# Kernel optimization log

Hardware: AMD Instinct MI355X
Metric: run time of the kernel (lower is better)

Reference implementation:

```python
import jax, jax.numpy as jnp
import numpy as np

B, N, E, D, H, HW, L = 16, 32, 256, 256, 8, 784, 4
DH = D // H
FF = 4 * D
BN = B * N
BE = B * E
SCALE = 1.0 / np.sqrt(DH)


def _ln(x, g, b):
    m = x.mean(-1, keepdims=True)
    v = ((x - m) ** 2).mean(-1, keepdims=True)
    return (x - m) * jax.lax.rsqrt(v + 1e-5) * g + b


def setup_inputs() -> dict:
    key = jax.random.key(0)
    ks = iter(jax.random.split(key, 64))
    def w(shape, s=0.05):
        return jax.random.normal(next(ks), shape, jnp.float32) * s
    inp = {
        'nodes': w((B, N, D), 1.0),
        'edges': w((B, E, D), 1.0),
        'images': w((B, HW, D), 1.0),
        'mask': jnp.zeros((B * H, N + E, HW), jnp.float32),
        'node_enc': w((BN, D), 1.0),
        'edge_enc': w((BE, D), 1.0),
        'ln1_g': jnp.ones((L, D), jnp.float32), 'ln1_b': jnp.zeros((L, D), jnp.float32),
        'Wqkv': w((L, D, 3 * D)), 'bqkv': jnp.zeros((L, 3 * D), jnp.float32),
        'Wo': w((L, D, D)), 'bo': jnp.zeros((L, D), jnp.float32),
        'ls1': jnp.full((L, D), 0.1, jnp.float32),
        'ln2_g': jnp.ones((L, D), jnp.float32), 'ln2_b': jnp.zeros((L, D), jnp.float32),
        'Wn1': w((L, D, D)), 'bn1': jnp.zeros((L, D), jnp.float32),
        'Wn2': w((L, D, D)), 'bn2': jnp.zeros((L, D), jnp.float32),
        'We': w((L, D, D)), 'be': jnp.zeros((L, D), jnp.float32),
        'attn_p': w((L, H, DH), 1.0),
        'Weo': w((L, D, D)), 'beo': jnp.zeros((L, D), jnp.float32),
        'Wno': w((L, D, D)), 'bno': jnp.zeros((L, D), jnp.float32),
        'ls2': jnp.full((L, D), 0.1, jnp.float32),
        'ln3_g': jnp.ones((L, D), jnp.float32), 'ln3_b': jnp.zeros((L, D), jnp.float32),
        'W1': w((L, D, FF)), 'b1': jnp.zeros((L, FF), jnp.float32),
        'W2': w((L, FF, D)), 'b2': jnp.zeros((L, D), jnp.float32),
        'ls3': jnp.full((L, D), 0.1, jnp.float32),
        'edge_index': jax.random.randint(next(ks), (2, BE), 0, BN, jnp.int32),
    }
    return inp


def reference(nodes, edges, images, mask, node_enc, edge_enc,
              ln1_g, ln1_b, Wqkv, bqkv, Wo, bo, ls1,
              ln2_g, ln2_b, Wn1, bn1, Wn2, bn2, We, be, attn_p, Weo, beo, Wno, bno, ls2,
              ln3_g, ln3_b, W1, b1, W2, b2, ls3, edge_index):
    idx0, idx1 = edge_index[0], edge_index[1]
    ne = jnp.concatenate([nodes, edges], axis=1)  # [B, N+E, D]
    mask4 = mask.reshape(B, H, N + E, HW)
    for l in range(L):
        # cross-attention ne -> images
        ne1n = _ln(ne, ln1_g[l], ln1_b[l])
        q = (ne1n @ Wqkv[l, :, :D] + bqkv[l, :D]).reshape(B, N + E, H, DH)
        k = (images @ Wqkv[l, :, D:2 * D] + bqkv[l, D:2 * D]).reshape(B, HW, H, DH)
        v = (images @ Wqkv[l, :, 2 * D:] + bqkv[l, 2 * D:]).reshape(B, HW, H, DH)
        scores = jnp.einsum('bqhd,bkhd->bhqk', q, k) * SCALE + mask4
        attn = jax.nn.softmax(scores, axis=-1)
        ctx = jnp.einsum('bhqk,bkhd->bqhd', attn, v).reshape(B, N + E, D)
        ne1 = ne + ls1[l] * (ctx @ Wo[l] + bo[l])
        # modified GAT on flattened graph
        ne2n = _ln(ne1, ln2_g[l], ln2_b[l])
        nodes_f = ne2n[:, :N].reshape(BN, D) + node_enc
        edges_f = ne2n[:, N:].reshape(BE, D) + edge_enc
        fn = (nodes_f @ Wn1[l] + bn1[l])[idx0]
        sn = (nodes_f @ Wn2[l] + bn2[l])[idx0]  # NOTE: original code uses edge_index[0] here too
        ep = edges_f @ We[l] + be[l]
        hidden = jax.nn.gelu(fn + sn + ep, approximate=False)  # [BE, D]
        pres = (hidden.reshape(BE, H, DH) * attn_p[l]).sum(-1)  # [BE, H]
        mseg = jax.ops.segment_max(pres, idx0, num_segments=BN)
        expv = jnp.exp(pres - mseg[idx0])
        denom = jax.ops.segment_sum(expv, idx0, num_segments=BN)
        alpha = expv / denom[idx0]  # scatter_softmax over destination nodes
        new_edges = hidden @ Weo[l] + beo[l]
        vals = (nodes_f[idx1] + new_edges) @ Wno[l] + bno[l]
        vals = vals.reshape(BE, H, DH) * alpha[..., None]
        new_nodes = jax.ops.segment_sum(vals.reshape(BE, D), idx0, num_segments=BN)
        gat = jnp.concatenate([new_nodes.reshape(B, N, D), new_edges.reshape(B, E, D)], axis=1)
        ne2 = ne1 + ls2[l] * gat
        # FFN
        ne3n = _ln(ne2, ln3_g[l], ln3_b[l])
        ffn = jax.nn.gelu(ne3n @ W1[l] + b1[l], approximate=False) @ W2[l] + b2[l]
        ne = ne2 + ls3[l] * ffn
    return ne
```

## Files before the change

kernel.cpp:

```cpp
#include <hip/hip_runtime.h>
#include <math.h>

static constexpr int B_  = 16;
static constexpr int N_  = 32;
static constexpr int E_  = 256;
static constexpr int D_  = 256;
static constexpr int H_  = 8;
static constexpr int HW_ = 784;
static constexpr int L_  = 4;
static constexpr int DH_ = 32;
static constexpr int FF_ = 1024;
static constexpr int BN_ = 512;
static constexpr int BE_ = 4096;
static constexpr int NE_ = 288;
static constexpr int ROWS_ = B_ * H_ * NE_;
#define SCALE_ 0.17677669529663687f

static constexpr size_t LAYER_W = 1114112;
static constexpr size_t OFF_Q   = 0;
static constexpr size_t OFF_K   = 65536;
static constexpr size_t OFF_WO  = 196608;
static constexpr size_t OFF_WN1 = 262144;
static constexpr size_t OFF_WE  = 393216;
static constexpr size_t OFF_WEO = 458752;
static constexpr size_t OFF_WNO = 524288;
static constexpr size_t OFF_W1  = 589824;
static constexpr size_t OFF_W2  = 851968;

typedef __attribute__((ext_vector_type(8))) short bf16x8;
typedef __attribute__((ext_vector_type(4))) float f32x4;

typedef __attribute__((address_space(1))) const unsigned int gas_uint;
typedef __attribute__((address_space(3))) unsigned int las_uint;

__device__ __forceinline__ void gload16(const unsigned short* g, unsigned short* lds) {
    __builtin_amdgcn_global_load_lds((gas_uint*)g, (las_uint*)lds, 16, 0, 0);
}

__device__ __forceinline__ float gelu_f(float x) {
    return 0.5f * x * (1.0f + erff(x * 0.7071067811865476f));
}

__device__ __forceinline__ unsigned short f2bf(float x) {
    unsigned u = __float_as_uint(x);
    u += 0x7FFFu + ((u >> 16) & 1u);
    return (unsigned short)(u >> 16);
}
__device__ __forceinline__ unsigned pack2bf(float a, float b) {
    return (unsigned)f2bf(a) | ((unsigned)f2bf(b) << 16);
}
__device__ __forceinline__ float bf2f(unsigned short u) {
    return __uint_as_float(((unsigned)u) << 16);
}


__global__ void concat_kernel(const float* __restrict__ nodes, const float* __restrict__ edges,
                              float* __restrict__ ne) {
    int tid = blockIdx.x * 256 + threadIdx.x;
    int d = tid & 255;
    int row = tid >> 8;
    int b = row / NE_, pos = row % NE_;
    float v = (pos < N_) ? nodes[(size_t)(b * N_ + pos) * D_ + d]
                         : edges[(size_t)(b * E_ + (pos - N_)) * D_ + d];
    ne[tid] = v;
}

__global__ void imgcast_kernel(const float* __restrict__ img, unsigned short* __restrict__ out) {
    int tid = blockIdx.x * 256 + threadIdx.x;
    const float* p = img + (size_t)tid * 8;
    float4 a = *(const float4*)(p);
    float4 b = *(const float4*)(p + 4);
    uint4 o = make_uint4(pack2bf(a.x, a.y), pack2bf(a.z, a.w),
                         pack2bf(b.x, b.y), pack2bf(b.z, b.w));
    *(uint4*)&out[(size_t)tid * 8] = o;
}

__device__ __forceinline__ float ln_from_val(float v, int d,
                                             const float* __restrict__ g, const float* __restrict__ bta,
                                             float* sh1, float* sh2) {
    float s = v, s2 = v * v;
    #pragma unroll
    for (int o = 32; o >= 1; o >>= 1) { s += __shfl_down(s, o); s2 += __shfl_down(s2, o); }
    int lane = d & 63, w = d >> 6;
    if (lane == 0) { sh1[w] = s; sh2[w] = s2; }
    __syncthreads();
    if (d == 0) {
        float a = sh1[0] + sh1[1] + sh1[2] + sh1[3];
        float c = sh2[0] + sh2[1] + sh2[2] + sh2[3];
        sh1[0] = a; sh2[0] = c;
    }
    __syncthreads();
    float mean = sh1[0] * (1.0f / D_);
    float var  = sh2[0] * (1.0f / D_) - mean * mean;
    float rstd = rsqrtf(var + 1e-5f);
    return (v - mean) * rstd * g[d] + bta[d];
}

__global__ __launch_bounds__(256) void ln_kernel(const float* __restrict__ x,
                                                 unsigned short* __restrict__ y,
                                                 const float* __restrict__ g,
                                                 const float* __restrict__ bta) {
    __shared__ float sh1[4], sh2[4];
    const int row = blockIdx.x, d = threadIdx.x;
    float v = x[(size_t)row * D_ + d];
    y[(size_t)row * D_ + d] = f2bf(ln_from_val(v, d, g, bta, sh1, sh2));
}

__global__ __launch_bounds__(256) void ln2enc_kernel(const float* __restrict__ x,
                                                     const float* __restrict__ g,
                                                     const float* __restrict__ bta,
                                                     const float* __restrict__ node_enc,
                                                     const float* __restrict__ edge_enc,
                                                     unsigned short* __restrict__ nodes_f,
                                                     unsigned short* __restrict__ edges_f) {
    __shared__ float sh1[4], sh2[4];
    const int row = blockIdx.x, d = threadIdx.x;
    float v = x[(size_t)row * D_ + d];
    float val = ln_from_val(v, d, g, bta, sh1, sh2);
    int b = row / NE_, pos = row % NE_;
    if (pos < N_) {
        int rn = b * N_ + pos;
        nodes_f[(size_t)rn * D_ + d] = f2bf(val + node_enc[(size_t)rn * D_ + d]);
    } else {
        int re = b * E_ + (pos - N_);
        edges_f[(size_t)re * D_ + d] = f2bf(val + edge_enc[(size_t)re * D_ + d]);
    }
}

__global__ __launch_bounds__(256) void gatres_ln_kernel(
    float* __restrict__ ne, const float* __restrict__ new_nodes,
    const float* __restrict__ new_edges, const float* __restrict__ ls2l,
    const float* __restrict__ g, const float* __restrict__ bta,
    unsigned short* __restrict__ lnb) {
    __shared__ float sh1[4], sh2[4];
    const int row = blockIdx.x, d = threadIdx.x;
    int b = row / NE_, pos = row % NE_;
    float gv = (pos < N_) ? new_nodes[(size_t)(b * N_ + pos) * D_ + d]
                          : new_edges[(size_t)(b * E_ + (pos - N_)) * D_ + d];
    float v = ne[(size_t)row * D_ + d] + ls2l[d] * gv;
    ne[(size_t)row * D_ + d] = v;
    lnb[(size_t)row * D_ + d] = f2bf(ln_from_val(v, d, g, bta, sh1, sh2));
}

__global__ __launch_bounds__(256) void wtrans_kernel(
    const float* __restrict__ Wqkv, const float* __restrict__ Wo,
    const float* __restrict__ Wn1,  const float* __restrict__ Wn2,
    const float* __restrict__ We,   const float* __restrict__ Weo,
    const float* __restrict__ Wno,  const float* __restrict__ W1,
    const float* __restrict__ W2,   unsigned short* __restrict__ wT)
{
    const int bid = blockIdx.x;
    const int l = bid / 1088;
    int tl = bid % 1088;
    const float* src; int ld, K, Nn; unsigned short* dst;
    if (tl < 576) {
        int mid = tl >> 6; tl &= 63;
        K = 256; Nn = 256;
        if (mid < 3) {
            src = Wqkv + (size_t)l * 256 * 768 + mid * 256; ld = 768;
            dst = wT + (size_t)l * LAYER_W + (size_t)mid * 65536;
        } else {
            const float* bases[6] = {Wo, Wn1, Wn2, We, Weo, Wno};
            src = bases[mid - 3] + (size_t)l * 65536; ld = 256;
            dst = wT + (size_t)l * LAYER_W + OFF_WO + (size_t)(mid - 3) * 65536;
        }
    } else if (tl < 832) {
        tl -= 576; K = 256; Nn = 1024;
        src = W1 + (size_t)l * 262144; ld = 1024;
        dst = wT + (size_t)l * LAYER_W + OFF_W1;
    } else {
        tl -= 832; K = 1024; Nn = 256;
        src = W2 + (size_t)l * 262144; ld = 256;
        dst = wT + (size_t)l * LAYER_W + OFF_W2;
    }
    const int ntn = Nn >> 5;
    const int k0 = (tl / ntn) << 5, n0 = (tl % ntn) << 5;
    __shared__ float ts[32][33];
    const int t = threadIdx.x;
    const int kl = t >> 5, nl = t & 31;
    #pragma unroll
    for (int rr = 0; rr < 4; ++rr)
        ts[kl + rr * 8][nl] = src[(size_t)(k0 + kl + rr * 8) * ld + n0 + nl];
    __syncthreads();
    const int onl = t >> 3, okl = (t & 7) << 2;
    ushort4 o;
    o.x = f2bf(ts[okl + 0][onl]); o.y = f2bf(ts[okl + 1][onl]);
    o.z = f2bf(ts[okl + 2][onl]); o.w = f2bf(ts[okl + 3][onl]);
    *(ushort4*)&dst[(size_t)(n0 + onl) * K + k0 + okl] = o;
}

template<int MODE, int OUTBF>
__global__ __launch_bounds__(256) void mgemm_kernel(
    const unsigned short* __restrict__ A, int lda,
    const unsigned short* __restrict__ Bt,
    const float* __restrict__ bias,
    const float* __restrict__ bias2,
    const float* __restrict__ res,
    const float* __restrict__ ls,
    void* __restrict__ Cv, int ldc, int K)
{
    __shared__ __align__(16) unsigned short As[64 * 64];
    __shared__ __align__(16) unsigned short Bs[64 * 64];
    const int m0 = blockIdx.y * 64, n0 = blockIdx.x * 64;
    const int t = threadIdx.x;
    const int l = t & 63, w = t >> 6;
    const int wr = (w >> 1) * 32, wc = (w & 1) * 32;
    const int frow = l & 15, kg = l >> 4;
    const int srow = w * 8 + (l >> 3);
    const int scolh = 8 * ((l & 7) ^ (l >> 3));
    const int ldsoff = w * 512;
    const int sw = (frow & 7) << 3;
    f32x4 acc[2][2];
    acc[0][0] = (f32x4){0.f,0.f,0.f,0.f}; acc[0][1] = acc[0][0];
    acc[1][0] = acc[0][0];                acc[1][1] = acc[0][0];
    for (int k0 = 0; k0 < K; k0 += 64) {
        const unsigned short* ga = A  + (size_t)(m0 + srow) * lda + k0 + scolh;
        const unsigned short* gb = Bt + (size_t)(n0 + srow) * K   + k0 + scolh;
        gload16(ga,                As + ldsoff);
        gload16(ga + 32 * lda,     As + ldsoff + 2048);
        gload16(gb,                Bs + ldsoff);
        gload16(gb + (size_t)32 * K, Bs + ldsoff + 2048);
        __syncthreads();
        #pragma unroll
        for (int kk = 0; kk < 2; ++kk) {
            const int off = (kk * 32 + kg * 8) ^ sw;
            bf16x8 af0 = *(const bf16x8*)&As[(wr + frow) * 64 + off];
            bf16x8 af1 = *(const bf16x8*)&As[(wr + 16 + frow) * 64 + off];
            bf16x8 bf0 = *(const bf16x8*)&Bs[(wc + frow) * 64 + off];
            bf16x8 bf1 = *(const bf16x8*)&Bs[(wc + 16 + frow) * 64 + off];
            acc[0][0] = __builtin_amdgcn_mfma_f32_16x16x32_bf16(af0, bf0, acc[0][0], 0, 0, 0);
            acc[0][1] = __builtin_amdgcn_mfma_f32_16x16x32_bf16(af0, bf1, acc[0][1], 0, 0, 0);
            acc[1][0] = __builtin_amdgcn_mfma_f32_16x16x32_bf16(af1, bf0, acc[1][0], 0, 0, 0);
            acc[1][1] = __builtin_amdgcn_mfma_f32_16x16x32_bf16(af1, bf1, acc[1][1], 0, 0, 0);
        }
        __syncthreads();
    }
    #pragma unroll
    for (int fr = 0; fr < 2; ++fr) {
        #pragma unroll
        for (int fc = 0; fc < 2; ++fc) {
            int n = n0 + wc + fc * 16 + frow;
            float bv = (bias2 != nullptr && n >= 256) ? bias2[n - 256] : bias[n];
            float lv = (MODE == 2) ? ls[n] : 0.f;
            #pragma unroll
            for (int rg = 0; rg < 4; ++rg) {
                int m = m0 + wr + fr * 16 + kg * 4 + rg;
                float vv = acc[fr][fc][rg] + bv;
                if (MODE == 1) vv = gelu_f(vv);
                if (MODE == 2) vv = res[(size_t)m * ldc + n] + lv * vv;
                if (OUTBF) ((unsigned short*)Cv)[(size_t)m * ldc + n] = f2bf(vv);
                else       ((float*)Cv)[(size_t)m * ldc + n] = vv;
            }
        }
    }
}

__global__ __launch_bounds__(128) void attn_part_kernel(
    const unsigned short* __restrict__ q, const unsigned short* __restrict__ kv,
    const float* __restrict__ mask,
    float* __restrict__ pm, float* __restrict__ pl, float* __restrict__ pO)
{
    const int bid = blockIdx.x;
    const int half = bid & 1;
    const int h = (bid >> 1) & 7;
    const int qt = (bid >> 4) % 9;
    const int b = (bid >> 4) / 9;
    const int q0 = qt * 32;
    const int t = threadIdx.x;
    const int w = t >> 6, l = t & 63;
    const int lr = l & 15, lg = l >> 4;
    const int cs = half ? 6 : 0;
    const int nc = half ? 7 : 6;

    __shared__ unsigned short Ks[2][64][40];
    __shared__ unsigned short Vs[2][32][72];
    __shared__ unsigned short Pl[2][16][72];

    bf16x8 qfrag = *(const bf16x8*)(q + ((size_t)(b * NE_ + q0 + w * 16 + lr)) * D_ + h * DH_ + lg * 8);

    const int kkey = t >> 1, kdh = (t & 1) * 16;
    const int vdh = (t & 7) * 4, vk0 = (t >> 3) * 2;
    const unsigned short* kbase = kv + ((size_t)b * HW_) * 512 + h * DH_;
    const unsigned short* vbase = kv + ((size_t)b * HW_) * 512 + 256 + h * DH_;
    const float* mbase = mask + ((size_t)(b * H_ + h) * NE_ + q0 + w * 16 + lg * 4) * (size_t)HW_;

    uint4 kq0, kq1;
    ushort4 va[2], vb4[2];
    float mreg[2][4][4];

    auto issue_kv = [&](int c0) {
        {
            int key = c0 + kkey;
            bool ok = key < HW_;
            const unsigned short* kp = kbase + (size_t)(ok ? key : 0) * 512 + kdh;
            kq0 = *(const uint4*)(kp);
            kq1 = *(const uint4*)(kp + 8);
            if (!ok) { kq0 = make_uint4(0,0,0,0); kq1 = kq0; }
        }
        #pragma unroll
        for (int r = 0; r < 2; ++r) {
            int key = c0 + vk0 + 32 * r;
            bool ok0 = key < HW_, ok1 = (key + 1) < HW_;
            const unsigned short* vp = vbase + (size_t)(ok0 ? key : 0) * 512 + vdh;
            va[r]  = *(const ushort4*)(vp);
            vb4[r] = *(const ushort4*)(vp + (ok1 ? 512 : 0));
            if (!ok0) va[r]  = make_ushort4(0,0,0,0);
            if (!ok1) vb4[r] = make_ushort4(0,0,0,0);
        }
    };
    auto write_kv = [&](int bufi) {
        *(uint4*)&Ks[bufi][kkey][kdh]     = kq0;
        *(uint4*)&Ks[bufi][kkey][kdh + 8] = kq1;
        #pragma unroll
        for (int r = 0; r < 2; ++r) {
            const unsigned short* a = (const unsigned short*)&va[r];
            const unsigned short* c = (const unsigned short*)&vb4[r];
            #pragma unroll
            for (int i = 0; i < 4; ++i)
                *(unsigned*)&Vs[bufi][vdh + i][vk0 + 32 * r] = (unsigned)a[i] | ((unsigned)c[i] << 16);
        }
    };
    auto issue_mask = [&](int c0, int set) {
        #pragma unroll
        for (int rg = 0; rg < 4; ++rg)
            #pragma unroll
            for (int fc = 0; fc < 4; ++fc) {
                int col = c0 + fc * 16 + lr;
                mreg[set][rg][fc] = (col < HW_) ? mbase[(size_t)rg * HW_ + col] : -1e30f;
            }
    };

    f32x4 oacc[2];
    oacc[0] = (f32x4){0.f, 0.f, 0.f, 0.f}; oacc[1] = oacc[0];
    float m_i[4] = {-INFINITY, -INFINITY, -INFINITY, -INFINITY};
    float l_i[4] = {0.f, 0.f, 0.f, 0.f};

    issue_kv(cs * 64);
    issue_mask(cs * 64, 0);
    write_kv(0);
    if (nc > 1) issue_mask(cs * 64 + 64, 1);
    __syncthreads();

    for (int i = 0; i < nc; ++i) {
        const int c0 = (cs + i) * 64;
        const int cb = i & 1, nb = cb ^ 1;
        const int set = i & 1;
        if (i + 1 < nc) issue_kv(c0 + 64);

        f32x4 sacc[4];
        #pragma unroll
        for (int fc = 0; fc < 4; ++fc) {
            sacc[fc] = (f32x4){0.f, 0.f, 0.f, 0.f};
            bf16x8 kf = *(const bf16x8*)&Ks[cb][fc * 16 + lr][lg * 8];
            sacc[fc] = __builtin_amdgcn_mfma_f32_16x16x32_bf16(qfrag, kf, sacc[fc], 0, 0, 0);
        }
        float s[4][4];
        #pragma unroll
        for (int fc = 0; fc < 4; ++fc)
            #pragma unroll
            for (int rg = 0; rg < 4; ++rg)
                s[fc][rg] = sacc[fc][rg] * SCALE_ + mreg[set][rg][fc];
        if (i + 2 < nc) issue_mask(c0 + 128, set);

        float mloc[4];
        #pragma unroll
        for (int rg = 0; rg < 4; ++rg)
            mloc[rg] = fmaxf(fmaxf(s[0][rg], s[1][rg]), fmaxf(s[2][rg], s[3][rg]));
        #pragma unroll
        for (int off = 1; off < 16; off <<= 1)
            #pragma unroll
            for (int rg = 0; rg < 4; ++rg)
                mloc[rg] = fmaxf(mloc[rg], __shfl_xor(mloc[rg], off));
        float scl[4], lloc[4];
        #pragma unroll
        for (int rg = 0; rg < 4; ++rg) {
            float mn = fmaxf(m_i[rg], mloc[rg]);
            scl[rg] = __expf(m_i[rg] - mn);
            m_i[rg] = mn;
        }
        #pragma unroll
        for (int rg = 0; rg < 4; ++rg) {
            float acc = 0.f;
            #pragma unroll
            for (int fc = 0; fc < 4; ++fc) {
                float p = __expf(s[fc][rg] - m_i[rg]);
                s[fc][rg] = p;
                acc += p;
            }
            lloc[rg] = acc;
        }
        #pragma unroll
        for (int off = 1; off < 16; off <<= 1)
            #pragma unroll
            for (int rg = 0; rg < 4; ++rg)
                lloc[rg] += __shfl_xor(lloc[rg], off);
        #pragma unroll
        for (int rg = 0; rg < 4; ++rg) {
            l_i[rg] = l_i[rg] * scl[rg] + lloc[rg];
            oacc[0][rg] *= scl[rg];
            oacc[1][rg] *= scl[rg];
        }

        #pragma unroll
        for (int fc = 0; fc < 4; ++fc)
            #pragma unroll
            for (int rg = 0; rg < 4; ++rg)
                Pl[w][lg * 4 + rg][fc * 16 + lr] = f2bf(s[fc][rg]);
        #pragma unroll
        for (int ks2 = 0; ks2 < 2; ++ks2) {
            bf16x8 pf = *(const bf16x8*)&Pl[w][lr][ks2 * 32 + lg * 8];
            #pragma unroll
            for (int d2 = 0; d2 < 2; ++d2) {
                bf16x8 vf = *(const bf16x8*)&Vs[cb][d2 * 16 + lr][ks2 * 32 + lg * 8];
                oacc[d2] = __builtin_amdgcn_mfma_f32_16x16x32_bf16(pf, vf, oacc[d2], 0, 0, 0);
            }
        }

        if (i + 1 < nc) {
            write_kv(nb);
            __syncthreads();
        }
    }

    const int rowbase = (b * H_ + h) * NE_ + q0 + w * 16 + lg * 4;
    #pragma unroll
    for (int rg = 0; rg < 4; ++rg) {
        size_t gr = (size_t)half * ROWS_ + rowbase + rg;
        #pragma unroll
        for (int d2 = 0; d2 < 2; ++d2)
            pO[gr * 32 + d2 * 16 + lr] = oacc[d2][rg];
        if (lr == 0) { pm[gr] = m_i[rg]; pl[gr] = l_i[rg]; }
    }
}

__global__ __launch_bounds__(256) void attn_combine_kernel(
    const float* __restrict__ pm, const float* __restrict__ pl,
    const float* __restrict__ pO, unsigned short* __restrict__ ctx)
{
    int tid = blockIdx.x * 256 + threadIdx.x;
    int row = tid >> 5, dh = tid & 31;
    float m0 = pm[row], m1 = pm[ROWS_ + row];
    float l0 = pl[row], l1 = pl[ROWS_ + row];
    float mm = fmaxf(m0, m1);
    float w0 = __expf(m0 - mm), w1 = __expf(m1 - mm);
    float L = l0 * w0 + l1 * w1;
    float o = (pO[(size_t)row * 32 + dh] * w0 + pO[((size_t)ROWS_ + row) * 32 + dh] * w1) / L;
    int bh = row / NE_, qq = row % NE_;
    int b = bh >> 3, h = bh & 7;
    ctx[((size_t)(b * NE_ + qq)) * D_ + h * DH_ + dh] = f2bf(o);
}


__global__ __launch_bounds__(256) void hidden_kernel(
    const float* __restrict__ gn12,
    unsigned short* __restrict__ hid, const int* __restrict__ idx0,
    const float* __restrict__ attn_p_l, float* __restrict__ pres) {
    int e = blockIdx.x;
    int d = threadIdx.x;
    int n = idx0[e];
    float x = bf2f(hid[(size_t)e * D_ + d]) + gn12[(size_t)n * 512 + d] + gn12[(size_t)n * 512 + 256 + d];
    float hv = gelu_f(x);
    hid[(size_t)e * D_ + d] = f2bf(hv);
    float pr = hv * attn_p_l[d];
    #pragma unroll
    for (int o = 1; o < 32; o <<= 1) pr += __shfl_xor(pr, o);
    if ((d & 31) == 0) pres[e * H_ + (d >> 5)] = pr;
}

__global__ void segsoft_kernel(const float* __restrict__ pres, const int* __restrict__ csr_off,
                               const int* __restrict__ csr_perm,
                               float* __restrict__ mseg, float* __restrict__ denom) {
    int tid = blockIdx.x * 256 + threadIdx.x;
    int n = tid >> 3, h = tid & 7;
    int s = csr_off[n], e2 = csr_off[n + 1];
    float mx = -INFINITY;
    for (int i = s; i < e2; ++i) mx = fmaxf(mx, pres[csr_perm[i] * H_ + h]);
    float sum = 0.f;
    for (int i = s; i < e2; ++i) sum += expf(pres[csr_perm[i] * H_ + h] - mx);
    mseg[tid] = mx;
    denom[tid] = sum;
}

__global__ void vin_kernel(const unsigned short* __restrict__ nodes_f,
                           const float* __restrict__ new_edges,
                           const int* __restrict__ idx1, unsigned short* __restrict__ vin) {
    int tid = blockIdx.x * 256 + threadIdx.x;
    int e = tid >> 8, d = tid & 255;
    vin[tid] = f2bf(bf2f(nodes_f[(size_t)idx1[e] * D_ + d]) + new_edges[tid]);
}

__global__ __launch_bounds__(256) void nodeagg_kernel(
    const float* __restrict__ vals, const float* __restrict__ pres,
    const float* __restrict__ mseg, const float* __restrict__ denom,
    const int* __restrict__ csr_off, const int* __restrict__ csr_perm,
    float* __restrict__ new_nodes) {
    int n = blockIdx.x;
    int d = threadIdx.x;
    int s = csr_off[n], e2 = csr_off[n + 1];
    int h = d >> 5;
    float ms = mseg[n * H_ + h];
    float rd = 1.0f / denom[n * H_ + h];
    float acc = 0.f;
    for (int i = s; i < e2; ++i) {
        int e = csr_perm[i];
        float a = expf(pres[e * H_ + h] - ms) * rd;
        acc += vals[(size_t)e * D_ + d] * a;
    }
    new_nodes[(size_t)n * D_ + d] = acc;
}


__global__ void zero_counts(int* counts) {
    int t = blockIdx.x * 256 + threadIdx.x;
    if (t < BN_) counts[t] = 0;
}

__global__ void csr_count(const int* __restrict__ idx0, int* __restrict__ counts) {
    int e = blockIdx.x * 256 + threadIdx.x;
    if (e < BE_) atomicAdd(&counts[idx0[e]], 1);
}

__global__ __launch_bounds__(512) void csr_scan(const int* __restrict__ counts, int* __restrict__ csr_off) {
    __shared__ int buf[BN_];
    int t = threadIdx.x;
    int c = counts[t];
    buf[t] = c;
    __syncthreads();
    for (int o = 1; o < BN_; o <<= 1) {
        int add = (t >= o) ? buf[t - o] : 0;
        __syncthreads();
        buf[t] += add;
        __syncthreads();
    }
    csr_off[t] = buf[t] - c;
    if (t == BN_ - 1) csr_off[BN_] = buf[t];
}

__global__ __launch_bounds__(64) void csr_fill(const int* __restrict__ idx0,
                                               const int* __restrict__ csr_off,
                                               int* __restrict__ csr_perm) {
    int n = blockIdx.x;
    int lane = threadIdx.x;
    int w = csr_off[n];
    for (int c0 = 0; c0 < BE_; c0 += 64) {
        int e = c0 + lane;
        bool m = (idx0[e] == n);
        unsigned long long bal = __ballot(m);
        if (m) {
            int pre = __popcll(bal & ((1ull << lane) - 1ull));
            csr_perm[w + pre] = e;
        }
        w += __popcll(bal);
    }
}


static void launch_mgemm(hipStream_t s, int mode, int outbf,
                         const unsigned short* A, int lda, const unsigned short* Bt,
                         const float* bias, const float* bias2, const float* res, const float* ls,
                         void* C, int ldc, int M, int N, int K) {
    dim3 g(N / 64, M / 64);
    if (mode == 0) {
        if (outbf) mgemm_kernel<0,1><<<g, 256, 0, s>>>(A, lda, Bt, bias, bias2, res, ls, C, ldc, K);
        else       mgemm_kernel<0,0><<<g, 256, 0, s>>>(A, lda, Bt, bias, bias2, res, ls, C, ldc, K);
    } else if (mode == 1) {
        mgemm_kernel<1,1><<<g, 256, 0, s>>>(A, lda, Bt, bias, bias2, res, ls, C, ldc, K);
    } else {
        mgemm_kernel<2,0><<<g, 256, 0, s>>>(A, lda, Bt, bias, bias2, res, ls, C, ldc, K);
    }
}

extern "C" void kernel_launch(void* const* d_in, const int* in_sizes, int n_in,
                              void* d_out, int out_size, void* d_ws, size_t ws_size,
                              hipStream_t stream) {
    const float* nodes    = (const float*)d_in[0];
    const float* edges    = (const float*)d_in[1];
    const float* images   = (const float*)d_in[2];
    const float* mask     = (const float*)d_in[3];
    const float* node_enc = (const float*)d_in[4];
    const float* edge_enc = (const float*)d_in[5];
    const float* ln1_g = (const float*)d_in[6];
    const float* ln1_b = (const float*)d_in[7];
    const float* Wqkv  = (const float*)d_in[8];
    const float* bqkv  = (const float*)d_in[9];
    const float* Wo    = (const float*)d_in[10];
    const float* bo    = (const float*)d_in[11];
    const float* ls1   = (const float*)d_in[12];
    const float* ln2_g = (const float*)d_in[13];
    const float* ln2_b = (const float*)d_in[14];
    const float* Wn1   = (const float*)d_in[15];
    const float* bn1   = (const float*)d_in[16];
    const float* Wn2   = (const float*)d_in[17];
    const float* bn2   = (const float*)d_in[18];
    const float* We    = (const float*)d_in[19];
    const float* be    = (const float*)d_in[20];
    const float* attn_p= (const float*)d_in[21];
    const float* Weo   = (const float*)d_in[22];
    const float* beo   = (const float*)d_in[23];
    const float* Wno   = (const float*)d_in[24];
    const float* bno   = (const float*)d_in[25];
    const float* ls2   = (const float*)d_in[26];
    const float* ln3_g = (const float*)d_in[27];
    const float* ln3_b = (const float*)d_in[28];
    const float* W1    = (const float*)d_in[29];
    const float* b1    = (const float*)d_in[30];
    const float* W2    = (const float*)d_in[31];
    const float* b2    = (const float*)d_in[32];
    const float* ls3   = (const float*)d_in[33];
    const int*   edge_index = (const int*)d_in[34];
    const int* idx0 = edge_index;
    const int* idx1 = edge_index + BE_;

    float* ne = (float*)d_out;

    float* cur = (float*)d_ws;
    auto alloc = [&](size_t nfl) { float* p = cur; cur += nfl; return p; };
    auto allocbf = [&](size_t nbf) { float* p = cur; cur += (nbf + 1) / 2; return (unsigned short*)p; };

    unsigned short* lnbuf   = allocbf((size_t)B_ * NE_ * D_);
    unsigned short* qb      = allocbf((size_t)B_ * NE_ * D_);
    unsigned short* kvb     = allocbf((size_t)B_ * HW_ * 512);
    unsigned short* ffnh    = kvb;
    unsigned short* imgbf   = allocbf((size_t)B_ * HW_ * D_);
    unsigned short* ctxb    = allocbf((size_t)B_ * NE_ * D_);
    unsigned short* nodes_f = allocbf((size_t)BN_ * D_);
    unsigned short* edges_f = allocbf((size_t)BE_ * D_);
    unsigned short* hid     = allocbf((size_t)BE_ * D_);
    unsigned short* vin     = allocbf((size_t)BE_ * D_);
    float* gn12     = alloc((size_t)BN_ * 512);
    float* pres     = alloc((size_t)BE_ * H_);
    float* mseg     = alloc((size_t)BN_ * H_);
    float* denom    = alloc((size_t)BN_ * H_);
    float* new_edges= alloc((size_t)BE_ * D_);
    float* valsb    = alloc((size_t)BE_ * D_);
    float* new_nodes= alloc((size_t)BN_ * D_);
    float* pm       = alloc((size_t)2 * ROWS_);
    float* pl       = alloc((size_t)2 * ROWS_);
    float* pO       = alloc((size_t)2 * ROWS_ * 32);
    int* counts   = (int*)cur; cur += BN_;
    int* csr_off  = (int*)cur; cur += BN_ + 4;
    int* csr_perm = (int*)cur; cur += BE_;
    cur = (float*)(((uintptr_t)cur + 255) & ~(uintptr_t)255);
    unsigned short* wT = (unsigned short*)cur;

    wtrans_kernel<<<4 * 1088, 256, 0, stream>>>(Wqkv, Wo, Wn1, Wn2, We, Weo, Wno, W1, W2, wT);
    imgcast_kernel<<<(B_ * HW_ * D_) / (256 * 8), 256, 0, stream>>>(images, imgbf);
    zero_counts<<<2, 256, 0, stream>>>(counts);
    csr_count<<<BE_ / 256, 256, 0, stream>>>(idx0, counts);
    csr_scan<<<1, 512, 0, stream>>>(counts, csr_off);
    csr_fill<<<BN_, 64, 0, stream>>>(idx0, csr_off, csr_perm);
    concat_kernel<<<(B_ * NE_ * D_) / 256, 256, 0, stream>>>(nodes, edges, ne);

    for (int l = 0; l < L_; ++l) {
        const unsigned short* wTl = wT + (size_t)l * LAYER_W;
        const float* bqkv_l = bqkv + (size_t)l * 3 * D_;

        ln_kernel<<<B_ * NE_, 256, 0, stream>>>(ne, lnbuf, ln1_g + l * D_, ln1_b + l * D_);
        launch_mgemm(stream, 0, 1, lnbuf, D_, wTl + OFF_Q, bqkv_l, nullptr, nullptr, nullptr,
                     qb, D_, B_ * NE_, D_, D_);
        launch_mgemm(stream, 0, 1, imgbf, D_, wTl + OFF_K, bqkv_l + D_, nullptr, nullptr, nullptr,
                     kvb, 512, B_ * HW_, 512, D_);
        attn_part_kernel<<<2304, 128, 0, stream>>>(qb, kvb, mask, pm, pl, pO);
        attn_combine_kernel<<<(ROWS_ * 32) / 256, 256, 0, stream>>>(pm, pl, pO, ctxb);
        launch_mgemm(stream, 2, 0, ctxb, D_, wTl + OFF_WO, bo + l * D_, nullptr, ne, ls1 + l * D_,
                     ne, D_, B_ * NE_, D_, D_);

        ln2enc_kernel<<<B_ * NE_, 256, 0, stream>>>(ne, ln2_g + l * D_, ln2_b + l * D_,
                                                    node_enc, edge_enc, nodes_f, edges_f);
        launch_mgemm(stream, 0, 0, nodes_f, D_, wTl + OFF_WN1, bn1 + l * D_, bn2 + l * D_,
                     nullptr, nullptr, gn12, 512, BN_, 512, D_);
        launch_mgemm(stream, 0, 1, edges_f, D_, wTl + OFF_WE, be + l * D_, nullptr, nullptr, nullptr,
                     hid, D_, BE_, D_, D_);
        hidden_kernel<<<BE_, 256, 0, stream>>>(gn12, hid, idx0, attn_p + (size_t)l * H_ * DH_, pres);
        segsoft_kernel<<<(BN_ * H_) / 256, 256, 0, stream>>>(pres, csr_off, csr_perm, mseg, denom);
        launch_mgemm(stream, 0, 0, hid, D_, wTl + OFF_WEO, beo + l * D_, nullptr, nullptr, nullptr,
                     new_edges, D_, BE_, D_, D_);
        vin_kernel<<<(BE_ * D_) / 256, 256, 0, stream>>>(nodes_f, new_edges, idx1, vin);
        launch_mgemm(stream, 0, 0, vin, D_, wTl + OFF_WNO, bno + l * D_, nullptr, nullptr, nullptr,
                     valsb, D_, BE_, D_, D_);
        nodeagg_kernel<<<BN_, 256, 0, stream>>>(valsb, pres, mseg, denom, csr_off, csr_perm, new_nodes);
        gatres_ln_kernel<<<B_ * NE_, 256, 0, stream>>>(ne, new_nodes, new_edges, ls2 + l * D_,
                                                       ln3_g + l * D_, ln3_b + l * D_, lnbuf);

        launch_mgemm(stream, 1, 1, lnbuf, D_, wTl + OFF_W1, b1 + l * FF_, nullptr, nullptr, nullptr,
                     ffnh, FF_, B_ * NE_, FF_, D_);
        launch_mgemm(stream, 2, 0, ffnh, FF_, wTl + OFF_W2, b2 + l * D_, nullptr, ne, ls3 + l * D_,
                     ne, D_, B_ * NE_, D_, FF_);
    }
}
```

Before: 704.4 us.

## Pre-convert mask to bf16 fragment layout once and drop split-KV attention

Adds a one-time premask kernel that converts the float32 attention mask to bf16, stored per block in the exact order each thread consumes it. All four layers' attention then read half the mask bytes with coalesced uint4 loads instead of scattered float loads. The attention kernel also stops splitting the key range in two, so each block walks all 13 key chunks and writes the normalised context directly, which removes the combine kernel and its partial buffers. The costs are half as many attention blocks (less parallelism), an extra pre-pass plus buffer, and bf16 rounding of mask values.

```diff
diff --git a/kernel.cpp b/kernel.cpp
--- a/kernel.cpp
+++ b/kernel.cpp
@@ -13,7 +13,8 @@
 static constexpr int BN_ = 512;
 static constexpr int BE_ = 4096;
 static constexpr int NE_ = 288;
-static constexpr int ROWS_ = B_ * H_ * NE_;
+static constexpr int NC_ = 13;
+static constexpr int NBLK_ = B_ * H_ * 9;
 #define SCALE_ 0.17677669529663687f
 
 static constexpr size_t LAYER_W = 1114112;
@@ -73,6 +74,47 @@
     uint4 o = make_uint4(pack2bf(a.x, a.y), pack2bf(a.z, a.w),
                          pack2bf(b.x, b.y), pack2bf(b.z, b.w));
     *(uint4*)&out[(size_t)tid * 8] = o;
+}
+
+__global__ __launch_bounds__(128) void premask_kernel(const float* __restrict__ mask,
+                                                      unsigned short* __restrict__ pmask) {
+    const int bid = blockIdx.x;
+    const int c = bid % NC_;
+    const int bq = bid / NC_;
+    const int h = bq & 7;
+    const int qt = (bq >> 3) % 9;
+    const int b = (bq >> 3) / 9;
+    const int q0 = qt * 32, c0 = c * 64;
+    __shared__ float ts[32][68];
+    const int t = threadIdx.x;
+    const int row = t >> 2, cg = (t & 3) * 16;
+    const float* mrow = mask + ((size_t)(b * H_ + h) * NE_ + q0 + row) * (size_t)HW_;
+    #pragma unroll
+    for (int i = 0; i < 4; ++i) {
+        int col = c0 + cg + i * 4;
+        float4 m4;
+        if (col + 4 <= HW_) {
+            m4 = *(const float4*)(mrow + col);
+        } else {
+            m4.x = (col + 0 < HW_) ? mrow[col + 0] : -1e30f;
+            m4.y = (col + 1 < HW_) ? mrow[col + 1] : -1e30f;
+            m4.z = (col + 2 < HW_) ? mrow[col + 2] : -1e30f;
+            m4.w = (col + 3 < HW_) ? mrow[col + 3] : -1e30f;
+        }
+        *(float4*)&ts[row][cg + i * 4] = m4;
+    }
+    __syncthreads();
+    const int w = t >> 6, lg = (t & 63) >> 4, lr = t & 15;
+    const int r0 = w * 16 + lg * 4;
+    unsigned u[8];
+    #pragma unroll
+    for (int rg = 0; rg < 4; ++rg) {
+        u[rg * 2 + 0] = pack2bf(ts[r0 + rg][0 * 16 + lr], ts[r0 + rg][1 * 16 + lr]);
+        u[rg * 2 + 1] = pack2bf(ts[r0 + rg][2 * 16 + lr], ts[r0 + rg][3 * 16 + lr]);
+    }
+    uint4* dst = (uint4*)(pmask + (size_t)bid * 2048 + t * 16);
+    dst[0] = make_uint4(u[0], u[1], u[2], u[3]);
+    dst[1] = make_uint4(u[4], u[5], u[6], u[7]);
 }
 
 __device__ __forceinline__ float ln_from_val(float v, int d,
@@ -255,22 +297,18 @@
     }
 }
 
-__global__ __launch_bounds__(128) void attn_part_kernel(
+__global__ __launch_bounds__(128) void attn_kernel(
     const unsigned short* __restrict__ q, const unsigned short* __restrict__ kv,
-    const float* __restrict__ mask,
-    float* __restrict__ pm, float* __restrict__ pl, float* __restrict__ pO)
+    const unsigned short* __restrict__ pmask, unsigned short* __restrict__ ctx)
 {
     const int bid = blockIdx.x;
-    const int half = bid & 1;
-    const int h = (bid >> 1) & 7;
-    const int qt = (bid >> 4) % 9;
-    const int b = (bid >> 4) / 9;
+    const int h = bid & 7;
+    const int qt = (bid >> 3) % 9;
+    const int b = (bid >> 3) / 9;
     const int q0 = qt * 32;
     const int t = threadIdx.x;
     const int w = t >> 6, l = t & 63;
     const int lr = l & 15, lg = l >> 4;
-    const int cs = half ? 6 : 0;
-    const int nc = half ? 7 : 6;
 
     __shared__ unsigned short Ks[2][64][40];
     __shared__ unsigned short Vs[2][32][72];
@@ -282,11 +320,11 @@
     const int vdh = (t & 7) * 4, vk0 = (t >> 3) * 2;
     const unsigned short* kbase = kv + ((size_t)b * HW_) * 512 + h * DH_;
     const unsigned short* vbase = kv + ((size_t)b * HW_) * 512 + 256 + h * DH_;
-    const float* mbase = mask + ((size_t)(b * H_ + h) * NE_ + q0 + w * 16 + lg * 4) * (size_t)HW_;
+    const uint4* mbase = (const uint4*)(pmask + (size_t)bid * NC_ * 2048 + t * 16);
 
     uint4 kq0, kq1;
     ushort4 va[2], vb4[2];
-    float mreg[2][4][4];
+    uint4 mc0, mc1, mn0, mn1;
 
     auto issue_kv = [&](int c0) {
         {
@@ -320,32 +358,22 @@
                 *(unsigned*)&Vs[bufi][vdh + i][vk0 + 32 * r] = (unsigned)a[i] | ((unsigned)c[i] << 16);
         }
     };
-    auto issue_mask = [&](int c0, int set) {
-        #pragma unroll
-        for (int rg = 0; rg < 4; ++rg)
-            #pragma unroll
-            for (int fc = 0; fc < 4; ++fc) {
-                int col = c0 + fc * 16 + lr;
-                mreg[set][rg][fc] = (col < HW_) ? mbase[(size_t)rg * HW_ + col] : -1e30f;
-            }
-    };
 
     f32x4 oacc[2];
     oacc[0] = (f32x4){0.f, 0.f, 0.f, 0.f}; oacc[1] = oacc[0];
     float m_i[4] = {-INFINITY, -INFINITY, -INFINITY, -INFINITY};
     float l_i[4] = {0.f, 0.f, 0.f, 0.f};
 
-    issue_kv(cs * 64);
-    issue_mask(cs * 64, 0);
+    issue_kv(0);
+    mc0 = mbase[0]; mc1 = mbase[1];
     write_kv(0);
-    if (nc > 1) issue_mask(cs * 64 + 64, 1);
+    mn0 = mbase[128]; mn1 = mbase[129];
     __syncthreads();
 
-    for (int i = 0; i < nc; ++i) {
-        const int c0 = (cs + i) * 64;
-        const int cb = i & 1, nb = cb ^ 1;
-        const int set = i & 1;
-        if (i + 1 < nc) issue_kv(c0 + 64);
+    for (int c = 0; c < NC_; ++c) {
+        const int c0 = c * 64;
+        const int cb = c & 1, nb = cb ^ 1;
+        if (c + 1 < NC_) issue_kv(c0 + 64);
 
         f32x4 sacc[4];
         #pragma unroll
@@ -355,12 +383,16 @@
             sacc[fc] = __builtin_amdgcn_mfma_f32_16x16x32_bf16(qfrag, kf, sacc[fc], 0, 0, 0);
         }
         float s[4][4];
-        #pragma unroll
-        for (int fc = 0; fc < 4; ++fc)
+        {
+            unsigned uw[8] = {mc0.x, mc0.y, mc0.z, mc0.w, mc1.x, mc1.y, mc1.z, mc1.w};
             #pragma unroll
-            for (int rg = 0; rg < 4; ++rg)
-                s[fc][rg] = sacc[fc][rg] * SCALE_ + mreg[set][rg][fc];
-        if (i + 2 < nc) issue_mask(c0 + 128, set);
+            for (int rg = 0; rg < 4; ++rg) {
+                s[0][rg] = sacc[0][rg] * SCALE_ + bf2f((unsigned short)(uw[rg * 2] & 0xffff));
+                s[1][rg] = sacc[1][rg] * SCALE_ + bf2f((unsigned short)(uw[rg * 2] >> 16));
+                s[2][rg] = sacc[2][rg] * SCALE_ + bf2f((unsigned short)(uw[rg * 2 + 1] & 0xffff));
+                s[3][rg] = sacc[3][rg] * SCALE_ + bf2f((unsigned short)(uw[rg * 2 + 1] >> 16));
+            }
+        }
 
         float mloc[4];
         #pragma unroll
@@ -416,38 +448,25 @@
             }
         }
 
-        if (i + 1 < nc) {
+        mc0 = mn0; mc1 = mn1;
+        if (c + 2 < NC_) {
+            mn0 = mbase[(c + 2) * 128];
+            mn1 = mbase[(c + 2) * 128 + 1];
+        }
+        if (c + 1 < NC_) {
             write_kv(nb);
             __syncthreads();
         }
     }
 
-    const int rowbase = (b * H_ + h) * NE_ + q0 + w * 16 + lg * 4;
+    unsigned short* cbase = ctx + ((size_t)(b * NE_ + q0 + w * 16 + lg * 4)) * D_ + h * DH_;
     #pragma unroll
     for (int rg = 0; rg < 4; ++rg) {
-        size_t gr = (size_t)half * ROWS_ + rowbase + rg;
+        float inv = 1.0f / l_i[rg];
         #pragma unroll
         for (int d2 = 0; d2 < 2; ++d2)
-            pO[gr * 32 + d2 * 16 + lr] = oacc[d2][rg];
-        if (lr == 0) { pm[gr] = m_i[rg]; pl[gr] = l_i[rg]; }
-    }
-}
-
-__global__ __launch_bounds__(256) void attn_combine_kernel(
-    const float* __restrict__ pm, const float* __restrict__ pl,
-    const float* __restrict__ pO, unsigned short* __restrict__ ctx)
-{
-    int tid = blockIdx.x * 256 + threadIdx.x;
-    int row = tid >> 5, dh = tid & 31;
-    float m0 = pm[row], m1 = pm[ROWS_ + row];
-    float l0 = pl[row], l1 = pl[ROWS_ + row];
-    float mm = fmaxf(m0, m1);
-    float w0 = __expf(m0 - mm), w1 = __expf(m1 - mm);
-    float L = l0 * w0 + l1 * w1;
-    float o = (pO[(size_t)row * 32 + dh] * w0 + pO[((size_t)ROWS_ + row) * 32 + dh] * w1) / L;
-    int bh = row / NE_, qq = row % NE_;
-    int b = bh >> 3, h = bh & 7;
-    ctx[((size_t)(b * NE_ + qq)) * D_ + h * DH_ + dh] = f2bf(o);
+            cbase[(size_t)rg * D_ + d2 * 16 + lr] = f2bf(oacc[d2][rg] * inv);
+    }
 }
 
 
@@ -627,6 +646,7 @@
     unsigned short* edges_f = allocbf((size_t)BE_ * D_);
     unsigned short* hid     = allocbf((size_t)BE_ * D_);
     unsigned short* vin     = allocbf((size_t)BE_ * D_);
+    unsigned short* pmaskb  = allocbf((size_t)NBLK_ * NC_ * 2048);
     float* gn12     = alloc((size_t)BN_ * 512);
     float* pres     = alloc((size_t)BE_ * H_);
     float* mseg     = alloc((size_t)BN_ * H_);
@@ -634,9 +654,6 @@
     float* new_edges= alloc((size_t)BE_ * D_);
     float* valsb    = alloc((size_t)BE_ * D_);
     float* new_nodes= alloc((size_t)BN_ * D_);
-    float* pm       = alloc((size_t)2 * ROWS_);
-    float* pl       = alloc((size_t)2 * ROWS_);
-    float* pO       = alloc((size_t)2 * ROWS_ * 32);
     int* counts   = (int*)cur; cur += BN_;
     int* csr_off  = (int*)cur; cur += BN_ + 4;
     int* csr_perm = (int*)cur; cur += BE_;
@@ -645,6 +662,7 @@
 
     wtrans_kernel<<<4 * 1088, 256, 0, stream>>>(Wqkv, Wo, Wn1, Wn2, We, Weo, Wno, W1, W2, wT);
     imgcast_kernel<<<(B_ * HW_ * D_) / (256 * 8), 256, 0, stream>>>(images, imgbf);
+    premask_kernel<<<NBLK_ * NC_, 128, 0, stream>>>(mask, pmaskb);
     zero_counts<<<2, 256, 0, stream>>>(counts);
     csr_count<<<BE_ / 256, 256, 0, stream>>>(idx0, counts);
     csr_scan<<<1, 512, 0, stream>>>(counts, csr_off);
@@ -660,8 +678,7 @@
                      qb, D_, B_ * NE_, D_, D_);
         launch_mgemm(stream, 0, 1, imgbf, D_, wTl + OFF_K, bqkv_l + D_, nullptr, nullptr, nullptr,
                      kvb, 512, B_ * HW_, 512, D_);
-        attn_part_kernel<<<2304, 128, 0, stream>>>(qb, kvb, mask, pm, pl, pO);
-        attn_combine_kernel<<<(ROWS_ * 32) / 256, 256, 0, stream>>>(pm, pl, pO, ctxb);
+        attn_kernel<<<NBLK_, 128, 0, stream>>>(qb, kvb, pmaskb, ctxb);
         launch_mgemm(stream, 2, 0, ctxb, D_, wTl + OFF_WO, bo + l * D_, nullptr, ne, ls1 + l * D_,
                      ne, D_, B_ * NE_, D_, D_);
 
```

Result: slower. 720.5 us (+2.3%).
